# Optimization experiments

Measured on AMD Instinct MI355X. Metric: run time of the kernel, lower is better.

## Reference

```python
import jax, jax.numpy as jnp
import numpy as np


def setup_inputs() -> dict:
    key = jax.random.key(0)
    k1, k2, k3, k4 = jax.random.split(key, 4)
    B, D_vis, E, N = 512, 4096, 1024, 512
    vf = jax.random.normal(k1, (B, D_vis), dtype=jnp.float32)
    p_lfs = jax.random.normal(k2, (B, E), dtype=jnp.float32)
    n_lfs = jax.random.normal(k3, (N, E), dtype=jnp.float32)
    W = jax.random.normal(k4, (E, D_vis), dtype=jnp.float32) * (1.0 / np.sqrt(D_vis))
    b = jnp.zeros((E,), dtype=jnp.float32)
    return {"vf": vf, "p_lfs": p_lfs, "n_lfs": n_lfs, "W": W, "b": b}


def _partial_order_sim(hypers, hypos):
    # -||relu(hypers - hypos)||_2 along last dim
    act = jax.nn.relu(hypers - hypos)
    return -jnp.sqrt(jnp.sum(act * act, axis=-1))


def reference(vf, p_lfs, n_lfs, W, b):
    # vf: [B, D_vis], W: [E, D_vis] -> vf_emb: [B, E]
    vf_emb = jnp.einsum("bd,ed->be", vf, W) + b
    # positive scores: [B]
    p_scores = _partial_order_sim(p_lfs, vf_emb)
    # negative scores, batched over B: n_lfs [N,E] vs vf_emb [B,E] -> [B,N]
    n_scores = _partial_order_sim(n_lfs[None, :, :], vf_emb[:, None, :])
    # score_stack: [B, 1+N]
    return jnp.concatenate([p_scores[:, None], n_scores], axis=1)
```

## Files before the change

kernel.cpp:

```cpp
#include <hip/hip_runtime.h>
#include <hip/hip_bf16.h>

constexpr int B = 512;
constexpr int D = 4096;
constexpr int E = 1024;
constexpr int N = 512;
constexpr int KS = 4;
constexpr int KC = D / KS;
constexpr int NSTEP = KC / 32;
constexpr int ES = 8;
constexpr int EC = E / ES;

typedef __attribute__((ext_vector_type(8))) short bf16x8;
typedef __attribute__((ext_vector_type(4))) float f32x4;
typedef float v2f __attribute__((ext_vector_type(2)));

typedef __attribute__((address_space(3))) void lds_void;
typedef const __attribute__((address_space(1))) void gbl_void;

__device__ __forceinline__ unsigned short f2bf(float f) {
    __hip_bfloat16 h = __float2bfloat16(f);
    return *reinterpret_cast<unsigned short*>(&h);
}

__global__ __launch_bounds__(256) void cvt_all(
    const float* __restrict__ vf, const float* __restrict__ W,
    unsigned short* __restrict__ vfB, unsigned short* __restrict__ WB)
{
    const int bid = blockIdx.x;
    const float* src;
    unsigned short* dst;
    int i;
    if (bid < 1024) { src = vf; dst = vfB; i = (bid * 256 + threadIdx.x) * 8; }
    else           { src = W;  dst = WB;  i = ((bid - 1024) * 256 + threadIdx.x) * 8; }
    float4 v0 = *(const float4*)(src + i);
    float4 v1 = *(const float4*)(src + i + 4);
    bf16x8 o;
    o[0] = (short)f2bf(v0.x); o[1] = (short)f2bf(v0.y);
    o[2] = (short)f2bf(v0.z); o[3] = (short)f2bf(v0.w);
    o[4] = (short)f2bf(v1.x); o[5] = (short)f2bf(v1.y);
    o[6] = (short)f2bf(v1.z); o[7] = (short)f2bf(v1.w);
    *(bf16x8*)(dst + i) = o;
}

__global__ __launch_bounds__(64) void gemm_lds(
    const unsigned short* __restrict__ vf,
    const unsigned short* __restrict__ W,
    float* __restrict__ part)
{
    __shared__ unsigned short sA[2][2048];
    __shared__ unsigned short sB[2][2048];

    const int L  = threadIdx.x;
    const int n0 = blockIdx.x * 64;
    const int m0 = blockIdx.y * 64;
    const int ks = blockIdx.z;

    const int subrow = L >> 2;
    const int qstg = (L & 3) ^ ((L >> 2) & 3) ^ ((L >> 4) & 3);
    const int kbeg = ks * KC;
    const unsigned short* aSrc[4];
    const unsigned short* bSrc[4];
    #pragma unroll
    for (int c = 0; c < 4; ++c) {
        aSrc[c] = vf + (size_t)(m0 + c * 16 + subrow) * D + kbeg + qstg * 8;
        bSrc[c] = W  + (size_t)(n0 + c * 16 + subrow) * D + kbeg + qstg * 8;
    }

    const int r16 = L & 15;
    const int quad = L >> 4;
    const int swz = quad ^ (r16 & 3) ^ ((r16 >> 2) & 3);
    const int aoff = r16 * 64 + swz * 16;

    f32x4 acc[4][4] = {};

    auto issue = [&](int step, int buf) {
        const size_t koff = (size_t)step * 32;
        #pragma unroll
        for (int c = 0; c < 4; ++c) {
            __builtin_amdgcn_global_load_lds(
                (gbl_void*)(aSrc[c] + koff),
                (lds_void*)((char*)&sA[buf][0] + c * 1024), 16, 0, 0);
            __builtin_amdgcn_global_load_lds(
                (gbl_void*)(bSrc[c] + koff),
                (lds_void*)((char*)&sB[buf][0] + c * 1024), 16, 0, 0);
        }
    };

    issue(0, 0);
    issue(1, 1);

    #pragma unroll 1
    for (int s = 0; s < NSTEP; ++s) {
        const int buf = s & 1;
        if (s == NSTEP - 1) __builtin_amdgcn_s_waitcnt(0x0F70);
        else                __builtin_amdgcn_s_waitcnt(0x0F78);

        bf16x8 af[4], bf_[4];
        #pragma unroll
        for (int i = 0; i < 4; ++i)
            af[i] = *(const bf16x8*)((const char*)&sA[buf][0] + i * 1024 + aoff);
        #pragma unroll
        for (int j = 0; j < 4; ++j)
            bf_[j] = *(const bf16x8*)((const char*)&sB[buf][0] + j * 1024 + aoff);

        #pragma unroll
        for (int i = 0; i < 4; ++i)
            #pragma unroll
            for (int j = 0; j < 4; ++j)
                acc[i][j] = __builtin_amdgcn_mfma_f32_16x16x32_bf16(
                    af[i], bf_[j], acc[i][j], 0, 0, 0);

        if (s + 2 < NSTEP) issue(s + 2, buf);
    }

    float* po = part + (size_t)ks * B * E;
    #pragma unroll
    for (int j = 0; j < 4; ++j) {
        const int col = n0 + j * 16 + r16;
        #pragma unroll
        for (int i = 0; i < 4; ++i) {
            const int row = m0 + i * 16 + quad * 4;
            #pragma unroll
            for (int r = 0; r < 4; ++r)
                po[(size_t)(row + r) * E + col] = acc[i][j][r];
        }
    }
}

__global__ __launch_bounds__(256) void reduce_emb(
    const float* __restrict__ part, const float* __restrict__ bias,
    float* __restrict__ emb)
{
    const int idx = (blockIdx.x * 256 + threadIdx.x) * 4;
    const int col = idx & (E - 1);
    float4 s = *(const float4*)(bias + col);
    #pragma unroll
    for (int ks = 0; ks < KS; ++ks) {
        float4 p = *(const float4*)(part + (size_t)ks * B * E + idx);
        s.x += p.x; s.y += p.y; s.z += p.z; s.w += p.w;
    }
    *(float4*)(emb + idx) = s;
}

__global__ __launch_bounds__(256, 2) void scores_part(
    const float* __restrict__ emb,
    const float* __restrict__ n_lfs,
    float* __restrict__ pn)
{
    constexpr int LDW = EC + 2;
    __shared__ float eS[64 * LDW];
    __shared__ float nS[64 * LDW];

    const int t  = threadIdx.x;
    const int n0 = blockIdx.x * 64;
    const int b0 = blockIdx.y * 64;
    const int e0 = blockIdx.z * EC;

    {
        const int row = t >> 2;
        const int cb  = (t & 3) * 32;
        const float* ep = emb   + (size_t)(b0 + row) * E + e0 + cb;
        const float* np = n_lfs + (size_t)(n0 + row) * E + e0 + cb;
        float* ed = &eS[row * LDW + cb];
        float* nd = &nS[row * LDW + cb];
        #pragma unroll
        for (int q = 0; q < 8; ++q) {
            float4 v = *(const float4*)(ep + q * 4);
            float4 w = *(const float4*)(np + q * 4);
            *(v2f*)(ed + q * 4)     = (v2f){v.x, v.y};
            *(v2f*)(ed + q * 4 + 2) = (v2f){v.z, v.w};
            *(v2f*)(nd + q * 4)     = (v2f){w.x, w.y};
            *(v2f*)(nd + q * 4 + 2) = (v2f){w.z, w.w};
        }
    }
    __syncthreads();

    const int ty = t >> 4;
    const int tx = t & 15;

    const v2f z = {0.f, 0.f};
    v2f acc[4][4] = {{z,z,z,z},{z,z,z,z},{z,z,z,z},{z,z,z,z}};

    #pragma unroll 4
    for (int e = 0; e < EC; e += 2) {
        v2f a[4], c[4];
        #pragma unroll
        for (int r = 0; r < 4; ++r)
            a[r] = *(const v2f*)&eS[(ty + 16 * r) * LDW + e];
        #pragma unroll
        for (int q = 0; q < 4; ++q)
            c[q] = *(const v2f*)&nS[(tx + 16 * q) * LDW + e];
        #pragma unroll
        for (int r = 0; r < 4; ++r)
            #pragma unroll
            for (int q = 0; q < 4; ++q) {
                v2f d = c[q] - a[r];
                d = __builtin_elementwise_max(d, z);
                acc[r][q] = __builtin_elementwise_fma(d, d, acc[r][q]);
            }
    }

    float* po = pn + (size_t)blockIdx.z * B * N;
    #pragma unroll
    for (int r = 0; r < 4; ++r) {
        const size_t ob = (size_t)(b0 + ty + 16 * r) * N;
        #pragma unroll
        for (int q = 0; q < 4; ++q)
            po[ob + n0 + tx + 16 * q] = acc[r][q].x + acc[r][q].y;
    }
}

__global__ __launch_bounds__(256) void scores_final(
    const float* __restrict__ pn,
    const float* __restrict__ emb,
    const float* __restrict__ p_lfs,
    float* __restrict__ out)
{
    const int t = threadIdx.x;
    if (blockIdx.x < 1024) {
        const int i = blockIdx.x * 256 + t;
        const int b = i >> 9;
        const int n = i & (N - 1);
        float s = 0.f;
        #pragma unroll
        for (int z = 0; z < ES; ++z)
            s += pn[(size_t)z * B * N + i];
        out[(size_t)b * 513 + 1 + n] = -sqrtf(s);
        return;
    }
    const int b0 = (blockIdx.x - 1024) * 32;
    const int r = t >> 3;
    const int g = t & 7;
    const float* pr = p_lfs + (size_t)(b0 + r) * E;
    const float* er = emb   + (size_t)(b0 + r) * E;
    float acc = 0.f;
    for (int e = g * 4; e < E; e += 32) {
        float4 p = *(const float4*)(pr + e);
        float4 v = *(const float4*)(er + e);
        float d;
        d = p.x - v.x; d = fmaxf(d, 0.f); acc = fmaf(d, d, acc);
        d = p.y - v.y; d = fmaxf(d, 0.f); acc = fmaf(d, d, acc);
        d = p.z - v.z; d = fmaxf(d, 0.f); acc = fmaf(d, d, acc);
        d = p.w - v.w; d = fmaxf(d, 0.f); acc = fmaf(d, d, acc);
    }
    #pragma unroll
    for (int off = 4; off; off >>= 1) acc += __shfl_down(acc, off, 8);
    if (g == 0) out[(size_t)(b0 + r) * 513] = -sqrtf(acc);
}

extern "C" void kernel_launch(void* const* d_in, const int* in_sizes, int n_in,
                              void* d_out, int out_size, void* d_ws, size_t ws_size,
                              hipStream_t stream) {
    const float* vf    = (const float*)d_in[0];
    const float* p_lfs = (const float*)d_in[1];
    const float* n_lfs = (const float*)d_in[2];
    const float* W     = (const float*)d_in[3];
    const float* bias  = (const float*)d_in[4];
    float* out = (float*)d_out;

    char* ws = (char*)d_ws;
    float*          pg  = (float*)ws;
    float*          pn  = (float*)ws;
    unsigned short* vfB = (unsigned short*)(ws + ((size_t)8 << 20));
    unsigned short* WB  = (unsigned short*)(ws + ((size_t)12 << 20));
    float*          emb = (float*)(ws + ((size_t)20 << 20));

    cvt_all<<<3072, 256, 0, stream>>>(vf, W, vfB, WB);

    dim3 g1(E / 64, B / 64, KS);
    gemm_lds<<<g1, 64, 0, stream>>>(vfB, WB, pg);

    reduce_emb<<<(B * E) / 1024, 256, 0, stream>>>(pg, bias, emb);

    dim3 g3(N / 64, B / 64, ES);
    scores_part<<<g3, 256, 0, stream>>>(emb, n_lfs, pn);

    scores_final<<<1024 + B / 32, 256, 0, stream>>>(pn, emb, p_lfs, out);
}
```

Measured before the change: 139.3 us.

## Deepen GEMM LDS prefetch pipeline to four stages and remap block order

```diff
diff --git a/kernel.cpp b/kernel.cpp
--- a/kernel.cpp
+++ b/kernel.cpp
@@ -10,6 +10,7 @@
 constexpr int NSTEP = KC / 32;
 constexpr int ES = 8;
 constexpr int EC = E / ES;
+constexpr int DEPTH = 4;
 
 typedef __attribute__((ext_vector_type(8))) short bf16x8;
 typedef __attribute__((ext_vector_type(4))) float f32x4;
@@ -48,13 +49,16 @@
     const unsigned short* __restrict__ W,
     float* __restrict__ part)
 {
-    __shared__ unsigned short sA[2][2048];
-    __shared__ unsigned short sB[2][2048];
+    __shared__ unsigned short sA[DEPTH][2048];
+    __shared__ unsigned short sB[DEPTH][2048];
 
     const int L  = threadIdx.x;
-    const int n0 = blockIdx.x * 64;
-    const int m0 = blockIdx.y * 64;
-    const int ks = blockIdx.z;
+
+    const int id = blockIdx.x + 16 * blockIdx.y + 128 * blockIdx.z;
+    const int l  = (id & 7) * 64 + (id >> 3);
+    const int ks = l >> 7;
+    const int n0 = ((((l >> 6) & 1) << 3) | (l & 7)) * 64;
+    const int m0 = ((l >> 3) & 7) * 64;
 
     const int subrow = L >> 2;
     const int qstg = (L & 3) ^ ((L >> 2) & 3) ^ ((L >> 4) & 3);
@@ -89,30 +93,37 @@
 
     issue(0, 0);
     issue(1, 1);
+    issue(2, 2);
+    issue(3, 3);
+
+    #define GSTEP(S, WC, ISS)                                                  \
+    {                                                                          \
+        const int buf_ = (S) & 3;                                              \
+        __builtin_amdgcn_s_waitcnt(WC);                                        \
+        bf16x8 af[4], bg[4];                                                   \
+        _Pragma("unroll")                                                      \
+        for (int i = 0; i < 4; ++i)                                            \
+            af[i] = *(const bf16x8*)((const char*)&sA[buf_][0] + i * 1024 + aoff); \
+        _Pragma("unroll")                                                      \
+        for (int j = 0; j < 4; ++j)                                            \
+            bg[j] = *(const bf16x8*)((const char*)&sB[buf_][0] + j * 1024 + aoff); \
+        _Pragma("unroll")                                                      \
+        for (int i = 0; i < 4; ++i)                                            \
+            _Pragma("unroll")                                                  \
+            for (int j = 0; j < 4; ++j)                                        \
+                acc[i][j] = __builtin_amdgcn_mfma_f32_16x16x32_bf16(           \
+                    af[i], bg[j], acc[i][j], 0, 0, 0);                         \
+        if (ISS) issue((S) + DEPTH, buf_);                                     \
+    }
 
     #pragma unroll 1
-    for (int s = 0; s < NSTEP; ++s) {
-        const int buf = s & 1;
-        if (s == NSTEP - 1) __builtin_amdgcn_s_waitcnt(0x0F70);
-        else                __builtin_amdgcn_s_waitcnt(0x0F78);
-
-        bf16x8 af[4], bf_[4];
-        #pragma unroll
-        for (int i = 0; i < 4; ++i)
-            af[i] = *(const bf16x8*)((const char*)&sA[buf][0] + i * 1024 + aoff);
-        #pragma unroll
-        for (int j = 0; j < 4; ++j)
-            bf_[j] = *(const bf16x8*)((const char*)&sB[buf][0] + j * 1024 + aoff);
-
-        #pragma unroll
-        for (int i = 0; i < 4; ++i)
-            #pragma unroll
-            for (int j = 0; j < 4; ++j)
-                acc[i][j] = __builtin_amdgcn_mfma_f32_16x16x32_bf16(
-                    af[i], bf_[j], acc[i][j], 0, 0, 0);
-
-        if (s + 2 < NSTEP) issue(s + 2, buf);
-    }
+    for (int s = 0; s < NSTEP - DEPTH; ++s)
+        GSTEP(s, 0x4F78, true);
+    GSTEP(NSTEP - 4, 0x4F78, false);
+    GSTEP(NSTEP - 3, 0x4F70, false);
+    GSTEP(NSTEP - 2, 0x0F78, false);
+    GSTEP(NSTEP - 1, 0x0F70, false);
+    #undef GSTEP
 
     float* po = part + (size_t)ks * B * E;
     #pragma unroll
```

After: 134.5 us. -3.4%, faster.
